# Kernel optimization log

Hardware: AMD Instinct MI355X
Metric: run time of the kernel (lower is better)

The kernel has to match this reference:

```python
import jax, jax.numpy as jnp
import numpy as np

B, T, D, H = 256, 1024, 64, 512
I = 1 + D          # time channel + data
O = 2 * D          # mean + std
STD_LB = 1e-3


def setup_inputs() -> dict:
    key = jax.random.key(0)
    ks = jax.random.split(key, 8)
    s = 0.05  # small init scale
    return {
        "xs": jax.random.normal(ks[0], (B, T, D), jnp.float32),
        "ts": jax.random.uniform(ks[1], (B, T, 1), jnp.float32),
        "W_ih": jax.random.normal(ks[2], (3 * H, I), jnp.float32) * s,
        "W_hh": jax.random.normal(ks[3], (3 * H, H), jnp.float32) * s,
        "b_ih": jax.random.normal(ks[4], (3 * H,), jnp.float32) * s,
        "b_hh": jax.random.normal(ks[5], (3 * H,), jnp.float32) * s,
        "W_dec": jax.random.normal(ks[6], (O, H), jnp.float32) * s,
        "b_dec": jax.random.normal(ks[7], (O,), jnp.float32) * s,
        "cutoff": 512,  # int(inference_start * seq_len) with inference_start=0.5
    }


def reference(xs, ts, W_ih, W_hh, b_ih, b_hh, W_dec, b_dec, cutoff):
    b, t_len, d = xs.shape
    h_dim = W_hh.shape[1]

    def step(carry, inp):
        h, x_hat = carry
        x_true, t_curr, t_idx = inp
        force = t_idx < cutoff  # teacher forcing for t < cutoff
        x_t = jnp.where(force, x_true, x_hat)                 # (B, D)
        x_in = jnp.concatenate([t_curr[:, :1], x_t], axis=-1)  # (B, 1+D)
        gi = x_in @ W_ih.T + b_ih                              # (B, 3H)
        gh = h @ W_hh.T + b_hh                                 # (B, 3H)
        i_r, i_z, i_n = jnp.split(gi, 3, axis=-1)
        h_r, h_z, h_n = jnp.split(gh, 3, axis=-1)
        r = jax.nn.sigmoid(i_r + h_r)
        z = jax.nn.sigmoid(i_z + h_z)
        n = jnp.tanh(i_n + r * h_n)
        h_new = (1.0 - z) * n + z * h                          # GRUCell update
        dec = h_new @ W_dec.T + b_dec                          # (B, 2D)
        mean = dec[:, :d]
        std = jnp.maximum(dec[:, d:], STD_LB)                  # clamp(min=std_lower_bound)
        out = jnp.concatenate([mean, std], axis=-1)
        return (h_new, mean), out

    h0 = jnp.zeros((b, h_dim), xs.dtype)
    init = (h0, xs[:, 0, :])
    xs_t = jnp.swapaxes(xs, 0, 1)   # (T, B, D)
    ts_t = jnp.swapaxes(ts, 0, 1)   # (T, B, 1)
    t_idx = jnp.arange(t_len)
    _, outs = jax.lax.scan(step, init, (xs_t, ts_t, t_idx))
    return jnp.swapaxes(outs, 0, 1)  # (B, T, 2D)
```

## Files before the change

kernel.cpp:

```cpp
#include <hip/hip_runtime.h>
#include <hip/hip_bf16.h>
#include <cstdint>
#include <cstddef>

typedef float f32x4 __attribute__((ext_vector_type(4)));
typedef short s16x8 __attribute__((ext_vector_type(8)));

#define B_  256
#define T_  1024
#define D_  64
#define H_  512
#define O_  128
#define JW  16
#define NG  48

#define SLABW64 49152

#define OFF_WGH   0
#define OFF_WGI2  49152
#define OFF_WGIX  98304
#define OFF_WDEC  104448
#define OFF_W0S   120832
#define OFF_C0S   121024
#define OFF_BIHS  121216
#define OFF_BHHS  121408
#define OFF_BDECS 121600
#define OFF_SCR   121728
#define SMEM_BYTES 122752

#define WS_WCOMB 0
#define WS_C0    1572864
#define WS_HSLAB 1579008
#define WS_HSZ   786432

__device__ inline f32x4 mfma16(s16x8 a, s16x8 b, f32x4 c) {
  return __builtin_amdgcn_mfma_f32_16x16x32_bf16(a, b, c, 0, 0, 0);
}

__device__ inline unsigned short f2bf(float f) {
  __hip_bfloat16 h = __float2bfloat16(f);
  unsigned short u;
  __builtin_memcpy(&u, &h, sizeof(u));
  return u;
}

__device__ inline s16x8 cvt8(const float* s) {
  union { unsigned short h[8]; s16x8 v; } p;
#pragma unroll
  for (int e = 0; e < 8; ++e) p.h[e] = f2bf(s[e]);
  return p.v;
}

__device__ inline s16x8 fragK512(const char* base, int n, int kc, int kg) {
  int byteoff = n * 1024 + (((kc * 64) + (kg * 16)) ^ ((n & 7) << 4));
  return *(const s16x8*)(base + byteoff);
}
__device__ inline s16x8 fragK64(const char* base, int n, int kc, int kg) {
  int byteoff = n * 128 + (((kc * 64) + (kg * 16)) ^ ((n & 7) << 4));
  return *(const s16x8*)(base + byteoff);
}

__device__ inline unsigned long long ld64a(const unsigned long long* p) {
  return __hip_atomic_load(p, __ATOMIC_RELAXED, __HIP_MEMORY_SCOPE_AGENT);
}
__device__ inline void st64a(unsigned long long* p, unsigned long long v) {
  __hip_atomic_store(p, v, __ATOMIC_RELAXED, __HIP_MEMORY_SCOPE_AGENT);
}

__device__ inline s16x8 unpack3(unsigned long long w0, unsigned long long w1,
                                unsigned long long w2) {
  union { unsigned short u[8]; s16x8 v; } ua;
  ua.u[0] = (unsigned short)w0; ua.u[1] = (unsigned short)(w0 >> 16);
  ua.u[2] = (unsigned short)(w0 >> 32);
  ua.u[3] = (unsigned short)w1; ua.u[4] = (unsigned short)(w1 >> 16);
  ua.u[5] = (unsigned short)(w1 >> 32);
  ua.u[6] = (unsigned short)w2; ua.u[7] = (unsigned short)(w2 >> 16);
  return ua.v;
}

#define LOADG(W, KC0)                                                     \
  {                                                                       \
    _Pragma("unroll") for (int k_ = 0; k_ < 4; ++k_) {                    \
      W[k_ * 3 + 0] = ld64a(rqL + ((KC0) + k_) * 192 + 0);                \
      W[k_ * 3 + 1] = ld64a(rqL + ((KC0) + k_) * 192 + 1);                \
      W[k_ * 3 + 2] = ld64a(rqL + ((KC0) + k_) * 192 + 2);                \
    }                                                                     \
  }

#define VERIFY(W, KC0)                                                    \
  {                                                                       \
    for (;;) {                                                            \
      unsigned long long bad_ = 0;                                        \
      _Pragma("unroll") for (int i_ = 0; i_ < 12; ++i_)                   \
          bad_ |= (W[i_] >> 48) ^ tge;                                    \
      if (!__any((int)(bad_ != 0))) break;                                \
      if (--budget <= 0) break;                                           \
      LOADG(W, KC0)                                                       \
    }                                                                     \
  }

#define UNPACKG(W, KC0)                                                   \
  {                                                                       \
    _Pragma("unroll") for (int k_ = 0; k_ < 4; ++k_)                      \
        a[(KC0) + k_] =                                                   \
            unpack3(W[k_ * 3], W[k_ * 3 + 1], W[k_ * 3 + 2]);             \
  }

__global__ void wcomb_kernel(const float* __restrict__ W_ih, const float* __restrict__ W_dec,
                             const float* __restrict__ b_ih, const float* __restrict__ b_dec,
                             unsigned short* __restrict__ Wcomb, float* __restrict__ c0) {
  __shared__ float arow[64];
  int i = blockIdx.x;
  int tid = threadIdx.x;
  if (tid < 64) arow[tid] = W_ih[(size_t)i * 65 + 1 + tid];
  __syncthreads();
  for (int j = tid; j < H_; j += 256) {
    float acc = 0.f;
#pragma unroll 8
    for (int d = 0; d < 64; ++d) acc += arow[d] * W_dec[(size_t)d * H_ + j];
    Wcomb[(size_t)i * H_ + j] = f2bf(acc);
  }
  if (tid == 0) {
    float acc = b_ih[i];
    for (int d = 0; d < 64; ++d) acc += arow[d] * b_dec[d];
    c0[i] = acc;
  }
}

__global__ __launch_bounds__(128, 1) void rnn_persist(
    const float* __restrict__ xs, const float* __restrict__ ts,
    const float* __restrict__ W_ih, const float* __restrict__ W_hh,
    const float* __restrict__ b_ih, const float* __restrict__ b_hh,
    const float* __restrict__ W_dec, const float* __restrict__ b_dec,
    const int* __restrict__ cutoffp,
    const unsigned short* __restrict__ Wcomb, const float* __restrict__ c0,
    unsigned long long* __restrict__ hslabE, float* __restrict__ out) {
  extern __shared__ char sm[];
  const int tid = threadIdx.x;
  const int wave = tid >> 6, lane = tid & 63;
  const int jl = lane & 15, kg = lane >> 4;
  const int cutoff = *cutoffp;

  const int bg = blockIdx.x & 7;
  const int cg = blockIdx.x >> 3;
  const int b0 = bg * 32;
  const int j0 = cg * JW;

  for (int u = tid; u < NG * 64; u += 128) {
    int r = u >> 6, blk = u & 63;
    int grow = (r >> 4) * H_ + j0 + (r & 15);
    s16x8 v = cvt8(W_hh + (size_t)grow * H_ + blk * 8);
    *(s16x8*)(sm + OFF_WGH + r * 1024 + ((blk * 16) ^ ((r & 7) << 4))) = v;
  }
  for (int u = tid; u < NG * 64; u += 128) {
    int r = u >> 6, blk = u & 63;
    int grow = (r >> 4) * H_ + j0 + (r & 15);
    s16x8 v = *(const s16x8*)(Wcomb + (size_t)grow * H_ + blk * 8);
    *(s16x8*)(sm + OFF_WGI2 + r * 1024 + ((blk * 16) ^ ((r & 7) << 4))) = v;
  }
  for (int u = tid; u < NG * 8; u += 128) {
    int r = u >> 3, blk = u & 7;
    int grow = (r >> 4) * H_ + j0 + (r & 15);
    s16x8 v = cvt8(W_ih + (size_t)grow * 65 + 1 + blk * 8);
    *(s16x8*)(sm + OFF_WGIX + r * 128 + ((blk * 16) ^ ((r & 7) << 4))) = v;
  }
  if (cg < 8) {
    for (int u = tid; u < 16 * 64; u += 128) {
      int r = u >> 6, blk = u & 63;
      s16x8 v = cvt8(W_dec + (size_t)(cg * 16 + r) * H_ + blk * 8);
      *(s16x8*)(sm + OFF_WDEC + r * 1024 + ((blk * 16) ^ ((r & 7) << 4))) = v;
    }
    if (tid < 16) ((float*)(sm + OFF_BDECS))[tid] = b_dec[cg * 16 + tid];
  }
  if (tid < NG) {
    int grow = (tid >> 4) * H_ + j0 + (tid & 15);
    ((float*)(sm + OFF_W0S))[tid]  = W_ih[(size_t)grow * 65];
    ((float*)(sm + OFF_C0S))[tid]  = c0[grow];
    ((float*)(sm + OFF_BIHS))[tid] = b_ih[grow];
    ((float*)(sm + OFF_BHHS))[tid] = b_hh[grow];
  }
  __syncthreads();

  const int mt = wave;
  const int rowg = b0 + mt * 16 + jl;
  const int hrow = b0 + mt * 16 + kg * 4;
  unsigned short* scr = (unsigned short*)(sm + OFF_SCR) + mt * 256;
  int budget = 200000;

  const size_t blkb = (size_t)(bg * 2 + mt) * 3072;
  const size_t laneoff = (size_t)kg * 48 + (size_t)jl * 3;
  const int wi0 = lane;
  const int wr0 = wi0 / 6, wk0 = wi0 % 6;
  const int wi1 = 64 + lane;
  const int wr1 = wi1 / 6, wk1 = wi1 % 6;

  const float* W0S  = (const float*)(sm + OFF_W0S);
  const float* C0S  = (const float*)(sm + OFF_C0S);
  const float* BIHS = (const float*)(sm + OFF_BIHS);
  const float* BHHS = (const float*)(sm + OFF_BHHS);
  const float w0r = W0S[jl],  w0z = W0S[16 + jl],  w0n = W0S[32 + jl];
  const float bir = BIHS[jl], biz = BIHS[16 + jl], bin_ = BIHS[32 + jl];
  const float c0r = C0S[jl],  c0z = C0S[16 + jl],  c0n = C0S[32 + jl];
  const float bhr = BHHS[jl], bhz = BHHS[16 + jl], bhn = BHHS[32 + jl];

  const bool do_dec = (cg < 8);
  const float bd = do_dec ? ((const float*)(sm + OFF_BDECS))[jl] : 0.f;
  const int oc = cg * 16 + jl;

  float hp[4] = {0.f, 0.f, 0.f, 0.f};

  for (int t = 0; t < T_; ++t) {
    const bool use_x = (t < cutoff) || (t == 0);
    const unsigned long long tge = (unsigned long long)(unsigned)t;
    const unsigned long long epw = (unsigned long long)(t + 1) << 48;
    const unsigned long long* rqL =
        hslabE + (size_t)((t + 1) & 1) * SLABW64 + blkb + laneoff;
    unsigned long long* wq = hslabE + (size_t)(t & 1) * SLABW64 + blkb;

    float tsv[4];
#pragma unroll
    for (int reg = 0; reg < 4; ++reg) tsv[reg] = ts[(size_t)(hrow + reg) * T_ + t];

    f32x4 g0{}, g1{}, g2{}, i0{}, i1{}, i2{};
    if (use_x) {
      s16x8 ax0 = cvt8(xs + ((size_t)rowg * T_ + t) * D_ + kg * 8);
      s16x8 ax1 = cvt8(xs + ((size_t)rowg * T_ + t) * D_ + 32 + kg * 8);
      i0 = mfma16(ax0, fragK64(sm + OFF_WGIX, jl,      0, kg), i0);
      i1 = mfma16(ax0, fragK64(sm + OFF_WGIX, 16 + jl, 0, kg), i1);
      i2 = mfma16(ax0, fragK64(sm + OFF_WGIX, 32 + jl, 0, kg), i2);
      i0 = mfma16(ax1, fragK64(sm + OFF_WGIX, jl,      1, kg), i0);
      i1 = mfma16(ax1, fragK64(sm + OFF_WGIX, 16 + jl, 1, kg), i1);
      i2 = mfma16(ax1, fragK64(sm + OFF_WGIX, 32 + jl, 1, kg), i2);
    }

    s16x8 a[16];
    if (t > 0) {
      unsigned long long w0b[12], w1b[12];
      LOADG(w0b, 0)
      LOADG(w1b, 4)

#define MFMA_CL(K0)                                                          \
      { _Pragma("unroll") for (int k_ = 0; k_ < 4; ++k_) {                   \
          int kc_ = (K0) + k_;                                               \
          g0 = mfma16(a[kc_], fragK512(sm + OFF_WGH, jl,      kc_, kg), g0); \
          g1 = mfma16(a[kc_], fragK512(sm + OFF_WGH, 16 + jl, kc_, kg), g1); \
          g2 = mfma16(a[kc_], fragK512(sm + OFF_WGH, 32 + jl, kc_, kg), g2); \
          if (!use_x) {                                                      \
            i0 = mfma16(a[kc_], fragK512(sm + OFF_WGI2, jl,      kc_, kg), i0); \
            i1 = mfma16(a[kc_], fragK512(sm + OFF_WGI2, 16 + jl, kc_, kg), i1); \
            i2 = mfma16(a[kc_], fragK512(sm + OFF_WGI2, 32 + jl, kc_, kg), i2); \
          } } }

      VERIFY(w0b, 0)
      UNPACKG(w0b, 0)
      LOADG(w0b, 8)
      MFMA_CL(0)
      VERIFY(w1b, 4)
      UNPACKG(w1b, 4)
      LOADG(w1b, 12)
      MFMA_CL(4)
      VERIFY(w0b, 8)
      UNPACKG(w0b, 8)
      MFMA_CL(8)
      VERIFY(w1b, 12)
      UNPACKG(w1b, 12)
      MFMA_CL(12)
#undef MFMA_CL
    }

    unsigned short hb[4];
#pragma unroll
    for (int reg = 0; reg < 4; ++reg) {
      const float xr = i0[reg] + tsv[reg] * w0r + (use_x ? bir : c0r) + g0[reg] + bhr;
      const float xz = i1[reg] + tsv[reg] * w0z + (use_x ? biz : c0z) + g1[reg] + bhz;
      const float an = i2[reg] + tsv[reg] * w0n + (use_x ? bin_ : c0n);
      const float gn = g2[reg] + bhn;
      const float r = 1.f / (1.f + __expf(-xr));
      const float z = 1.f / (1.f + __expf(-xz));
      const float e2 = __expf(2.f * (an + r * gn));
      const float n = 1.f - 2.f / (e2 + 1.f);
      const float hn = (1.f - z) * n + z * hp[reg];
      hp[reg] = hn;
      hb[reg] = f2bf(hn);
    }

#pragma unroll
    for (int reg = 0; reg < 4; ++reg) scr[(kg * 4 + reg) * 16 + jl] = hb[reg];
    asm volatile("s_waitcnt lgkmcnt(0)" ::: "memory");
    __builtin_amdgcn_sched_barrier(0);
    {
      const int fg = wk0 / 3, pos = wk0 % 3;
      const int cb = fg * 8 + pos * 3;
      unsigned long long v =
          (unsigned long long)scr[wr0 * 16 + cb] |
          ((unsigned long long)scr[wr0 * 16 + cb + 1] << 16) |
          (pos < 2 ? ((unsigned long long)scr[wr0 * 16 + cb + 2] << 32) : 0ull) |
          epw;
      st64a(wq + (size_t)(cg >> 1) * 192 +
                (size_t)((cg & 1) * 2 + fg) * 48 + (size_t)wr0 * 3 + pos, v);
    }
    if (lane < 32) {
      const int fg = wk1 / 3, pos = wk1 % 3;
      const int cb = fg * 8 + pos * 3;
      unsigned long long v =
          (unsigned long long)scr[wr1 * 16 + cb] |
          ((unsigned long long)scr[wr1 * 16 + cb + 1] << 16) |
          (pos < 2 ? ((unsigned long long)scr[wr1 * 16 + cb + 2] << 32) : 0ull) |
          epw;
      st64a(wq + (size_t)(cg >> 1) * 192 +
                (size_t)((cg & 1) * 2 + fg) * 48 + (size_t)wr1 * 3 + pos, v);
    }

    if (do_dec && t > 0) {
      f32x4 dacc{};
#pragma unroll
      for (int kc = 0; kc < 16; ++kc)
        dacc = mfma16(a[kc], fragK512(sm + OFF_WDEC, jl, kc, kg), dacc);
#pragma unroll
      for (int reg = 0; reg < 4; ++reg) {
        float vv = dacc[reg] + bd;
        if (oc >= D_) vv = fmaxf(vv, 0.001f);
        out[((size_t)(hrow + reg) * T_ + (t - 1)) * O_ + oc] = vv;
      }
    }
  }

  if (do_dec) {
    const unsigned long long tge = (unsigned long long)(unsigned)T_;
    const unsigned long long* rqL =
        hslabE + (size_t)((T_ - 1) & 1) * SLABW64 + blkb + laneoff;
    f32x4 dacc{};
    unsigned long long wv[12];
    s16x8 a[16];
#pragma unroll
    for (int grp = 0; grp < 4; ++grp) {
      LOADG(wv, grp * 4)
      VERIFY(wv, grp * 4)
      UNPACKG(wv, grp * 4)
#pragma unroll
      for (int k = 0; k < 4; ++k) {
        int kc = grp * 4 + k;
        dacc = mfma16(a[kc], fragK512(sm + OFF_WDEC, jl, kc, kg), dacc);
      }
    }
#pragma unroll
    for (int reg = 0; reg < 4; ++reg) {
      float vv = dacc[reg] + bd;
      if (oc >= D_) vv = fmaxf(vv, 0.001f);
      out[((size_t)(hrow + reg) * T_ + (T_ - 1)) * O_ + oc] = vv;
    }
  }
}

extern "C" void kernel_launch(void* const* d_in, const int* in_sizes, int n_in,
                              void* d_out, int out_size, void* d_ws, size_t ws_size,
                              hipStream_t stream) {
  const float* xs    = (const float*)d_in[0];
  const float* ts    = (const float*)d_in[1];
  const float* W_ih  = (const float*)d_in[2];
  const float* W_hh  = (const float*)d_in[3];
  const float* b_ih  = (const float*)d_in[4];
  const float* b_hh  = (const float*)d_in[5];
  const float* W_dec = (const float*)d_in[6];
  const float* b_dec = (const float*)d_in[7];
  const int* cutoff  = (const int*)d_in[8];
  float* out = (float*)d_out;

  char* ws = (char*)d_ws;
  unsigned short* Wcomb      = (unsigned short*)(ws + WS_WCOMB);
  float* c0                  = (float*)(ws + WS_C0);
  unsigned long long* hslabE = (unsigned long long*)(ws + WS_HSLAB);

  hipMemsetAsync(ws + WS_HSLAB, 0, WS_HSZ, stream);
  wcomb_kernel<<<1536, 256, 0, stream>>>(W_ih, W_dec, b_ih, b_dec, Wcomb, c0);
  hipFuncSetAttribute(reinterpret_cast<const void*>(rnn_persist),
                      hipFuncAttributeMaxDynamicSharedMemorySize, SMEM_BYTES);
  rnn_persist<<<256, 128, SMEM_BYTES, stream>>>(xs, ts, W_ih, W_hh, b_ih, b_hh,
                                                W_dec, b_dec, cutoff, Wcomb, c0,
                                                hslabE, out);
}
```

Before: 4.903 ms.

## Prefetch next-step hidden state early and stage decoder output for vector stores

```diff
diff --git a/kernel.cpp b/kernel.cpp
--- a/kernel.cpp
+++ b/kernel.cpp
@@ -26,7 +26,8 @@
 #define OFF_BHHS  121408
 #define OFF_BDECS 121600
 #define OFF_SCR   121728
-#define SMEM_BYTES 122752
+#define OFF_SCRF  122752
+#define SMEM_BYTES 124928
 
 #define WS_WCOMB 0
 #define WS_C0    1572864
@@ -185,6 +186,7 @@
   const int rowg = b0 + mt * 16 + jl;
   const int hrow = b0 + mt * 16 + kg * 4;
   unsigned short* scr = (unsigned short*)(sm + OFF_SCR) + mt * 256;
+  float* scrF = (float*)(sm + OFF_SCRF) + mt * 272;
   int budget = 200000;
 
   const size_t blkb = (size_t)(bg * 2 + mt) * 3072;
@@ -208,13 +210,14 @@
   const int oc = cg * 16 + jl;
 
   float hp[4] = {0.f, 0.f, 0.f, 0.f};
+  s16x8 a[16];
+  unsigned long long w0b[12], w1b[12];
+  const unsigned long long* rqL = nullptr;
 
   for (int t = 0; t < T_; ++t) {
     const bool use_x = (t < cutoff) || (t == 0);
     const unsigned long long tge = (unsigned long long)(unsigned)t;
     const unsigned long long epw = (unsigned long long)(t + 1) << 48;
-    const unsigned long long* rqL =
-        hslabE + (size_t)((t + 1) & 1) * SLABW64 + blkb + laneoff;
     unsigned long long* wq = hslabE + (size_t)(t & 1) * SLABW64 + blkb;
 
     float tsv[4];
@@ -233,12 +236,7 @@
       i2 = mfma16(ax1, fragK64(sm + OFF_WGIX, 32 + jl, 1, kg), i2);
     }
 
-    s16x8 a[16];
     if (t > 0) {
-      unsigned long long w0b[12], w1b[12];
-      LOADG(w0b, 0)
-      LOADG(w1b, 4)
-
 #define MFMA_CL(K0)                                                          \
       { _Pragma("unroll") for (int k_ = 0; k_ < 4; ++k_) {                   \
           int kc_ = (K0) + k_;                                               \
@@ -311,6 +309,12 @@
                 (size_t)((cg & 1) * 2 + fg) * 48 + (size_t)wr1 * 3 + pos, v);
     }
 
+    if (t + 1 < T_) {
+      rqL = hslabE + (size_t)(t & 1) * SLABW64 + blkb + laneoff;
+      LOADG(w0b, 0)
+      LOADG(w1b, 4)
+    }
+
     if (do_dec && t > 0) {
       f32x4 dacc{};
 #pragma unroll
@@ -320,18 +324,24 @@
       for (int reg = 0; reg < 4; ++reg) {
         float vv = dacc[reg] + bd;
         if (oc >= D_) vv = fmaxf(vv, 0.001f);
-        out[((size_t)(hrow + reg) * T_ + (t - 1)) * O_ + oc] = vv;
+        scrF[(kg * 4 + reg) * 17 + jl] = vv;
+      }
+      asm volatile("s_waitcnt lgkmcnt(0)" ::: "memory");
+      __builtin_amdgcn_sched_barrier(0);
+      {
+        const int row = lane >> 2, seg = lane & 3;
+        f32x4 ov = *(const f32x4*)(scrF + row * 17 + seg * 4);
+        *(f32x4*)(out + ((size_t)(b0 + mt * 16 + row) * T_ + (t - 1)) * O_ +
+                  cg * 16 + seg * 4) = ov;
       }
     }
   }
 
   if (do_dec) {
     const unsigned long long tge = (unsigned long long)(unsigned)T_;
-    const unsigned long long* rqL =
-        hslabE + (size_t)((T_ - 1) & 1) * SLABW64 + blkb + laneoff;
+    rqL = hslabE + (size_t)((T_ - 1) & 1) * SLABW64 + blkb + laneoff;
     f32x4 dacc{};
     unsigned long long wv[12];
-    s16x8 a[16];
 #pragma unroll
     for (int grp = 0; grp < 4; ++grp) {
       LOADG(wv, grp * 4)
@@ -347,7 +357,15 @@
     for (int reg = 0; reg < 4; ++reg) {
       float vv = dacc[reg] + bd;
       if (oc >= D_) vv = fmaxf(vv, 0.001f);
-      out[((size_t)(hrow + reg) * T_ + (T_ - 1)) * O_ + oc] = vv;
+      scrF[(kg * 4 + reg) * 17 + jl] = vv;
+    }
+    asm volatile("s_waitcnt lgkmcnt(0)" ::: "memory");
+    __builtin_amdgcn_sched_barrier(0);
+    {
+      const int row = lane >> 2, seg = lane & 3;
+      f32x4 ov = *(const f32x4*)(scrF + row * 17 + seg * 4);
+      *(f32x4*)(out + ((size_t)(b0 + mt * 16 + row) * T_ + (T_ - 1)) * O_ +
+                cg * 16 + seg * 4) = ov;
     }
   }
 }
```

After: 7.186 ms. 46.6% more time.
